# Kernel tuning notes

Measured on AMD Instinct MI355X. Metric: run time of the kernel, lower is better.

Reference implementation:

```python
import jax, jax.numpy as jnp
import numpy as np

N, E, E_LBL = 50000, 800000, 200000
D_IN, H = 128, 128


def setup_inputs() -> dict:
    key = jax.random.key(0)
    ks = jax.random.split(key, 12)
    s = 0.05
    return {
        "x": jax.random.normal(ks[0], (N, D_IN), jnp.float32),
        "edge_index": jax.random.randint(ks[1], (2, E), 0, N, jnp.int64),
        "edge_label_index": jax.random.randint(ks[2], (2, E_LBL), 0, N, jnp.int64),
        "pre_w": jax.random.normal(ks[3], (D_IN, H), jnp.float32) * s,
        "pre_b": jax.random.normal(ks[4], (H,), jnp.float32) * s,
        "Wx": jax.random.normal(ks[5], (3, 2, H, H), jnp.float32) * s,  # gates z,r,h x cheb orders T0,T1
        "bx": jax.random.normal(ks[6], (3, H), jnp.float32) * s,
        "Wh": jax.random.normal(ks[7], (3, 2, H, H), jnp.float32) * s,
        "bh": jax.random.normal(ks[8], (3, H), jnp.float32) * s,
        "post_w": jax.random.normal(ks[9], (H, 2), jnp.float32) * s,
        "post_b": jax.random.normal(ks[10], (2,), jnp.float32) * s,
    }


def reference(x, edge_index, edge_label_index, pre_w, pre_b, Wx, bx, Wh, bh, post_w, post_b):
    n = x.shape[0]
    src, dst = edge_index[0], edge_index[1]

    # Scaled Chebyshev Laplacian (sym norm, lambda_max=2): L_hat = -D^{-1/2} A D^{-1/2}
    # (diagonal of L_hat is exactly 0, so only off-diagonal edge terms remain).
    deg = jax.ops.segment_sum(jnp.ones_like(src, dtype=x.dtype), src, num_segments=n)
    dinv = jnp.where(deg > 0, jax.lax.rsqrt(jnp.maximum(deg, 1.0)), 0.0)
    w = -(dinv[src] * dinv[dst])  # [E]

    def lap(v):  # L_hat @ v : gather src rows, weight, scatter-add at dst
        return jax.ops.segment_sum(w[:, None] * v[src], dst, num_segments=n)

    def cheb(v, Lv, W2, b):  # ChebConv K=2: T0(v)@W0 + T1(v)@W1 + b
        return v @ W2[0] + Lv @ W2[1] + b

    # pre: Linear(input_dim -> hidden)
    Xh = x @ pre_w + pre_b  # [N, H]
    LX = lap(Xh)

    # GConvGRU single step, H0 = 0
    Hc = jnp.zeros_like(Xh)
    LH = lap(Hc)
    Z = jax.nn.sigmoid(cheb(Xh, LX, Wx[0], bx[0]) + cheb(Hc, LH, Wh[0], bh[0]))
    R = jax.nn.sigmoid(cheb(Xh, LX, Wx[1], bx[1]) + cheb(Hc, LH, Wh[1], bh[1]))
    HR = Hc * R
    LHR = lap(HR)
    Ht = jnp.tanh(cheb(Xh, LX, Wx[2], bx[2]) + cheb(HR, LHR, Wh[2], bh[2]))
    Hc = Z * Hc + (1.0 - Z) * Ht

    h = jax.nn.relu(Hc)
    # link decoder: gather endpoints, hadamard, Linear(H->2), sum over logits
    hprod = h[edge_label_index[0]] * h[edge_label_index[1]]  # [E_lbl, H]
    out = hprod @ post_w + post_b  # [E_lbl, 2]
    return jnp.sum(out, axis=-1)  # [E_lbl]
```

## Files before the change

### kernel.cpp

```cpp
#include <hip/hip_runtime.h>
#include <math.h>


#define RND 2048
#define SORT_CAP 1536
#define CAPB 6144

typedef __attribute__((ext_vector_type(4))) float f32x4;
typedef __attribute__((ext_vector_type(8))) short short8;

static __device__ __forceinline__ unsigned short f2b(float f) {
  union { float f; unsigned u; } v; v.f = f;
  unsigned r = (v.u + 0x7fffu + ((v.u >> 16) & 1u)) >> 16;
  return (unsigned short)r;
}
static __device__ __forceinline__ float b2f(unsigned short s) {
  union { unsigned u; float f; } v; v.u = ((unsigned)s) << 16;
  return v.f;
}

__global__ __launch_bounds__(256) void prep_kernel(const float* __restrict__ pre_w, const float* __restrict__ Wx,
                                                   const float* __restrict__ bx, const float* __restrict__ bh,
                                                   const float* __restrict__ post_w, const float* __restrict__ post_b,
                                                   unsigned short* __restrict__ Bt1c, unsigned short* __restrict__ Btc2,
                                                   float* __restrict__ fb2, float* __restrict__ pwsum,
                                                   int* __restrict__ binPos) {
  int e = blockIdx.x * 256 + threadIdx.x;
  if (e < 512) binPos[e] = (e & 255) * CAPB;
  if (e < 16384) {
    int kc = e >> 12, r = e & 4095, col = r >> 5, kk = r & 31;
    Bt1c[e] = f2b(pre_w[(kc * 32 + kk) * 128 + col]);
  }
  int e2 = e - 16384;
  if (e2 >= 0 && e2 < 65536) {
    int kc = e2 >> 13, r = e2 & 8191, cB = r >> 5, kk = r & 31;
    int k = kc * 32 + kk, half = k >> 7, ki = k & 127;
    int cb = cB >> 7, r7 = cB & 127, nw6 = r7 >> 6, u2 = r7 & 63;
    int g = (u2 >= 32) ? 2 : 0, hcol = cb * 64 + nw6 * 32 + (u2 & 31);
    Btc2[e2] = f2b(Wx[((g * 2 + half) * 128 + ki) * 128 + hcol]);
  }
  int e3 = e - (16384 + 65536);
  if (e3 >= 0 && e3 < 256) {
    int cB = e3;
    int cb = cB >> 7, r7 = cB & 127, nw6 = r7 >> 6, u2 = r7 & 63;
    int g = (u2 >= 32) ? 2 : 0, hcol = cb * 64 + nw6 * 32 + (u2 & 31);
    fb2[cB] = bx[g * 128 + hcol] + bh[g * 128 + hcol];
  }
  int e4 = e - (16384 + 65536 + 256);
  if (e4 >= 0 && e4 < 128) pwsum[e4] = post_w[2 * e4] + post_w[2 * e4 + 1];
  if (e4 == 128) pwsum[128] = post_b[0] + post_b[1];
}

union SMemU {
  struct { unsigned short As[128 * 40]; unsigned short Bs[128 * 40]; } g;
  struct { unsigned ent[RND]; int hist[256], lstart[256], lofs[256], gbase[256], wsum[4];
           unsigned char ebin[RND], sb[RND]; } s;
};

__global__ __launch_bounds__(256) void mega1_kernel(const float* __restrict__ x,
                                                    const unsigned short* __restrict__ Bt1c,
                                                    const float* __restrict__ pre_b,
                                                    unsigned short* __restrict__ Xq,
                                                    const int* __restrict__ ei, int* __restrict__ binPos,
                                                    unsigned* __restrict__ bins,
                                                    unsigned char* __restrict__ sbins,
                                                    int N, int E, int RB) {
  __shared__ SMemU sm;
  const int t = threadIdx.x;

  if ((int)blockIdx.x < RB) {
    unsigned short* As = sm.g.As;
    unsigned short* Bs = sm.g.Bs;
    const int r0 = blockIdx.x * 128;
    const int w = t >> 6, lane = t & 63;
    const int m = lane & 15, q = lane >> 4;
    const int mw = (w >> 1) * 64, nw = (w & 1) * 64;

    f32x4 acc[4][4];
#pragma unroll
    for (int i = 0; i < 4; ++i)
#pragma unroll
      for (int j = 0; j < 4; ++j) acc[i][j] = {0.f, 0.f, 0.f, 0.f};

    const int arow = t >> 1, aseg = t & 1;
    const bool arow_ok = (r0 + arow) < N;
    const float* asrc0 = &x[(size_t)(r0 + arow) * 128 + aseg * 16];

    float4 cav[4]; short8 cbv0, cbv1;
    {
      if (arow_ok) {
#pragma unroll
        for (int i = 0; i < 4; ++i) cav[i] = *(const float4*)(asrc0 + i * 4);
      } else {
#pragma unroll
        for (int i = 0; i < 4; ++i) cav[i] = make_float4(0.f, 0.f, 0.f, 0.f);
      }
      const char* src = (const char*)Bt1c + t * 32;
      cbv0 = *(const short8*)src;
      cbv1 = *(const short8*)(src + 16);
    }

    for (int kc = 0; kc < 4; ++kc) {
      __syncthreads();
      {
        short8 t0, t1;
#pragma unroll
        for (int i = 0; i < 2; ++i) {
          t0[i * 4 + 0] = (short)f2b(cav[i].x); t0[i * 4 + 1] = (short)f2b(cav[i].y);
          t0[i * 4 + 2] = (short)f2b(cav[i].z); t0[i * 4 + 3] = (short)f2b(cav[i].w);
          t1[i * 4 + 0] = (short)f2b(cav[i + 2].x); t1[i * 4 + 1] = (short)f2b(cav[i + 2].y);
          t1[i * 4 + 2] = (short)f2b(cav[i + 2].z); t1[i * 4 + 3] = (short)f2b(cav[i + 2].w);
        }
        *(short8*)&As[arow * 40 + aseg * 16] = t0;
        *(short8*)&As[arow * 40 + aseg * 16 + 8] = t1;
        int bcol = t >> 1, boff = (t & 1) * 16;
        *(short8*)&Bs[bcol * 40 + boff] = cbv0;
        *(short8*)&Bs[bcol * 40 + boff + 8] = cbv1;
      }
      float4 nav[4]; short8 nbv0, nbv1;
      if (kc < 3) {
        if (arow_ok) {
          const float* src = asrc0 + (kc + 1) * 32;
#pragma unroll
          for (int i = 0; i < 4; ++i) nav[i] = *(const float4*)(src + i * 4);
        } else {
#pragma unroll
          for (int i = 0; i < 4; ++i) nav[i] = make_float4(0.f, 0.f, 0.f, 0.f);
        }
        const char* src = (const char*)Bt1c + (size_t)(kc + 1) * 8192 + t * 32;
        nbv0 = *(const short8*)src;
        nbv1 = *(const short8*)(src + 16);
      }
      __syncthreads();
      short8 af[4], bf[4];
#pragma unroll
      for (int i = 0; i < 4; ++i) af[i] = *(const short8*)&As[(mw + i * 16 + m) * 40 + q * 8];
#pragma unroll
      for (int j = 0; j < 4; ++j) bf[j] = *(const short8*)&Bs[(nw + j * 16 + m) * 40 + q * 8];
#pragma unroll
      for (int i = 0; i < 4; ++i)
#pragma unroll
        for (int j = 0; j < 4; ++j)
          acc[i][j] = __builtin_amdgcn_mfma_f32_16x16x32_bf16(af[i], bf[j], acc[i][j], 0, 0, 0);
      if (kc < 3) {
#pragma unroll
        for (int i = 0; i < 4; ++i) cav[i] = nav[i];
        cbv0 = nbv0; cbv1 = nbv1;
      }
    }

#pragma unroll
    for (int i = 0; i < 4; ++i) {
      int rb2 = r0 + mw + i * 16 + q * 4;
#pragma unroll
      for (int j = 0; j < 4; ++j) {
        int col = nw + j * 16 + m;
        float bias = pre_b[col];
#pragma unroll
        for (int r = 0; r < 4; ++r) {
          int row = rb2 + r;
          if (row < N) Xq[(size_t)row * 128 + col] = f2b(acc[i][j][r] + bias);
        }
      }
    }
    return;
  }

  unsigned* ent = sm.s.ent;
  unsigned char* ebin = sm.s.ebin;
  unsigned char* sb = sm.s.sb;
  int* hist = sm.s.hist;
  int* lstart = sm.s.lstart;
  int* lofs = sm.s.lofs;
  int* gbase = sm.s.gbase;
  int* wsum = sm.s.wsum;
  const int sbid = (int)blockIdx.x - RB;
  const int snum = (int)gridDim.x - RB;
  const int w = t >> 6, lane = t & 63;
  for (long long base = (long long)sbid * RND; base < E; base += (long long)snum * RND) {
    int cnt = (int)(((long long)E - base < RND) ? (E - base) : RND);
    if (t < 256) hist[t] = 0;
    __syncthreads();
    int my_s[8], my_d[8];
#pragma unroll
    for (int u = 0; u < 8; ++u) {
      int i = u * 256 + t;
      my_s[u] = -1;
      if (i < cnt) {
        int idx = (int)base + i;
        my_s[u] = ei[idx];
        my_d[u] = ei[E + idx];
        atomicAdd(&hist[my_d[u] >> 8], 1);
      }
    }
    __syncthreads();
    {
      int h = hist[t];
      hist[t] = 0;
      int v = h;
#pragma unroll
      for (int dd = 1; dd < 64; dd <<= 1) { int uu = __shfl_up(v, dd); if (lane >= dd) v += uu; }
      if (lane == 63) wsum[w] = v;
      __syncthreads();
      int woff = 0;
#pragma unroll
      for (int ww = 0; ww < 3; ++ww) if (ww < w) woff += wsum[ww];
      int excl = v - h + woff;
      lstart[t] = excl; lofs[t] = excl;
      if (h > 0) gbase[t] = atomicAdd(&binPos[t], h);
    }
    __syncthreads();
#pragma unroll
    for (int u = 0; u < 8; ++u) {
      if (my_s[u] >= 0) {
        int b = my_d[u] >> 8;
        int p = atomicAdd(&lofs[b], 1);
        ent[p] = (unsigned)my_s[u] | ((unsigned)(my_d[u] & 255) << 16);
        ebin[p] = (unsigned char)b;
        atomicAdd(&hist[my_s[u] >> 8], 1);
      }
    }
    __syncthreads();
    for (int i = t; i < cnt; i += 256) {
      int b = ebin[i];
      int pos = gbase[b] + (i - lstart[b]);
      if (pos < (b + 1) * CAPB) bins[pos] = ent[i];
    }
    __syncthreads();
    {
      int h = hist[t];
      int v = h;
#pragma unroll
      for (int dd = 1; dd < 64; dd <<= 1) { int uu = __shfl_up(v, dd); if (lane >= dd) v += uu; }
      if (lane == 63) wsum[w] = v;
      __syncthreads();
      int woff = 0;
#pragma unroll
      for (int ww = 0; ww < 3; ++ww) if (ww < w) woff += wsum[ww];
      int excl = v - h + woff;
      lstart[t] = excl; lofs[t] = excl;
      if (h > 0) gbase[t] = atomicAdd(&binPos[256 + t], h);
    }
    __syncthreads();
#pragma unroll
    for (int u = 0; u < 8; ++u) {
      if (my_s[u] >= 0) {
        int b = my_s[u] >> 8;
        int p = atomicAdd(&lofs[b], 1);
        sb[p] = (unsigned char)(my_s[u] & 255);
        ebin[p] = (unsigned char)b;
      }
    }
    __syncthreads();
    for (int i = t; i < cnt; i += 256) {
      int b = ebin[i];
      int pos = gbase[b] + (i - lstart[b]);
      if (pos < (b + 1) * CAPB) sbins[pos] = sb[i];
    }
    __syncthreads();
  }
}

__global__ __launch_bounds__(256) void deghist_kernel(const unsigned char* __restrict__ sbins,
                                                      const int* __restrict__ binPos,
                                                      int* __restrict__ deg, int N) {
  __shared__ int h[256];
  const int t = threadIdx.x;
  const int bin = blockIdx.x;
  h[t] = 0;
  __syncthreads();
  int T2 = binPos[256 + bin] - bin * CAPB;
  if (T2 > CAPB) T2 = CAPB;
  const unsigned char* __restrict__ p = sbins + (size_t)bin * CAPB;
  for (int i = t; i < T2; i += 256) atomicAdd(&h[p[i]], 1);
  __syncthreads();
  int node = bin * 256 + t;
  if (node < N) deg[node] = h[t];
}

__global__ __launch_bounds__(512) void lap_bin_kernel(const unsigned short* __restrict__ Xq,
                                                      unsigned short* __restrict__ LXc,
                                                      const unsigned* __restrict__ bins,
                                                      const int* __restrict__ binPos,
                                                      const int* __restrict__ deg, int N) {
  __shared__ unsigned eLDS[CAPB];
  __shared__ unsigned short sortS[SORT_CAP];
  __shared__ float sortW[SORT_CAP];
  __shared__ int hist[64], start[64], off[64];
  const int t = threadIdx.x;
  const int bin = blockIdx.x >> 2, qt = blockIdx.x & 3;
  const int lo = bin * CAPB;
  int T = binPos[bin] - lo;
  if (T > CAPB) T = CAPB;
  const unsigned* __restrict__ ebase = &bins[lo];
  if (t < 64) hist[t] = 0;
  __syncthreads();
  for (int i = t; i < T; i += 512) {
    unsigned e = ebase[i];
    eLDS[i] = e;
    int dl = (e >> 16) & 255;
    if ((dl >> 6) == qt) atomicAdd(&hist[dl & 63], 1);
  }
  __syncthreads();
  if (t < 64) {
    int h = hist[t];
    int v = h;
#pragma unroll
    for (int d = 1; d < 64; d <<= 1) {
      int u = __shfl_up(v, d);
      if (t >= d) v += u;
    }
    start[t] = v - h;
    off[t] = v - h;
  }
  __syncthreads();
  for (int i = t; i < T; i += 512) {
    unsigned e = eLDS[i];
    int dl = (e >> 16) & 255;
    if ((dl >> 6) == qt) {
      int s = (int)(e & 0xFFFFu);
      int p = atomicAdd(&off[dl & 63], 1);
      if (p < SORT_CAP) {
        int dg = deg[s];
        sortS[p] = (unsigned short)s;
        sortW[p] = dg > 0 ? rsqrtf((float)dg) : 0.0f;
      }
    }
  }
  __syncthreads();
  const int wv = t >> 6, lane = t & 63;
  for (int n = wv; n < 64; n += 8) {
    int node = bin * 256 + qt * 64 + n;
    if (node >= N) break;
    int st = start[n], cnum = hist[n];
    float ax = 0.f, ay = 0.f;
    for (int j = 0; j < cnum; j += 8) {
      unsigned v[8]; float ws[8];
#pragma unroll
      for (int u = 0; u < 8; ++u) {
        int idx = j + u;
        int s = 0; float w = 0.f;
        if (idx < cnum) { s = sortS[st + idx]; w = sortW[st + idx]; }
        ws[u] = w;
        v[u] = *(const unsigned*)((const char*)Xq + (size_t)s * 256 + lane * 4);
      }
#pragma unroll
      for (int u = 0; u < 8; ++u) {
        union { unsigned u32; float f; } fl, fh;
        fl.u32 = v[u] << 16; fh.u32 = v[u] & 0xffff0000u;
        ax += ws[u] * fl.f;
        ay += ws[u] * fh.f;
      }
    }
    int dgn = deg[node];
    float wd = dgn > 0 ? -rsqrtf((float)dgn) : 0.0f;
    unsigned o = (unsigned)f2b(ax * wd) | ((unsigned)f2b(ay * wd) << 16);
    *(unsigned*)((char*)LXc + (size_t)node * 256 + lane * 4) = o;
  }
}

__global__ __launch_bounds__(256) void gemm2_mfma(const unsigned short* __restrict__ Xq,
                                                  const unsigned short* __restrict__ LXc,
                                                  const unsigned short* __restrict__ Btc2,
                                                  const float* __restrict__ fb2,
                                                  unsigned short* __restrict__ hb, int N) {
  __shared__ unsigned short As[128 * 40];
  __shared__ unsigned short Bs[128 * 40];
  const int t = threadIdx.x;
  const int rb = blockIdx.x >> 1, cb = blockIdx.x & 1;
  const int r0 = rb * 128;
  const int w = t >> 6, lane = t & 63;
  const int m = lane & 15, q = lane >> 4;
  const int mw = (w >> 1) * 64, nw = (w & 1) * 64;

  f32x4 acc[4][4];
#pragma unroll
  for (int i = 0; i < 4; ++i)
#pragma unroll
    for (int j = 0; j < 4; ++j) acc[i][j] = {0.f, 0.f, 0.f, 0.f};

  const int arow = t >> 1;
  const int aoff = (t & 1) * 32;
  const char* aXq = (const char*)Xq + (size_t)(r0 + arow) * 256 + aoff;
  const char* aLX = (const char*)LXc + (size_t)(r0 + arow) * 256 + aoff;
  const char* bsrc0 = (const char*)Btc2 + (size_t)cb * 8192 + t * 32;

  short8 cav0, cav1, cbv0, cbv1;
  cav0 = *(const short8*)aXq;
  cav1 = *(const short8*)(aXq + 16);
  cbv0 = *(const short8*)bsrc0;
  cbv1 = *(const short8*)(bsrc0 + 16);

  for (int kc = 0; kc < 8; ++kc) {
    __syncthreads();
    *(short8*)&As[arow * 40 + (aoff >> 1)] = cav0;
    *(short8*)&As[arow * 40 + (aoff >> 1) + 8] = cav1;
    {
      int bcol = t >> 1, boff = (t & 1) * 16;
      *(short8*)&Bs[bcol * 40 + boff] = cbv0;
      *(short8*)&Bs[bcol * 40 + boff + 8] = cbv1;
    }
    short8 nav0, nav1, nbv0, nbv1;
    if (kc < 7) {
      int kn = kc + 1;
      const char* asrc = (kn < 4) ? (aXq + kn * 64) : (aLX + (kn - 4) * 64);
      nav0 = *(const short8*)asrc;
      nav1 = *(const short8*)(asrc + 16);
      const char* bsrc = bsrc0 + (size_t)kn * 16384;
      nbv0 = *(const short8*)bsrc;
      nbv1 = *(const short8*)(bsrc + 16);
    }
    __syncthreads();
    short8 af[4], bf[4];
#pragma unroll
    for (int i = 0; i < 4; ++i) af[i] = *(const short8*)&As[(mw + i * 16 + m) * 40 + q * 8];
#pragma unroll
    for (int j = 0; j < 4; ++j) bf[j] = *(const short8*)&Bs[(nw + j * 16 + m) * 40 + q * 8];
#pragma unroll
    for (int i = 0; i < 4; ++i)
#pragma unroll
      for (int j = 0; j < 4; ++j)
        acc[i][j] = __builtin_amdgcn_mfma_f32_16x16x32_bf16(af[i], bf[j], acc[i][j], 0, 0, 0);
    if (kc < 7) { cav0 = nav0; cav1 = nav1; cbv0 = nbv0; cbv1 = nbv1; }
  }

#pragma unroll
  for (int i = 0; i < 4; ++i) {
    int rbase = r0 + mw + i * 16 + q * 4;
#pragma unroll
    for (int jz = 0; jz < 2; ++jz) {
      int cBz = cb * 128 + nw + jz * 16 + m;
      int hc = cb * 64 + (nw >> 1) + jz * 16 + m;
      float bz = fb2[cBz], bt = fb2[cBz + 32];
#pragma unroll
      for (int r = 0; r < 4; ++r) {
        int row = rbase + r;
        if (row < N) {
          float zp = acc[i][jz][r] + bz;
          float tp = acc[i][jz + 2][r] + bt;
          float zs = 1.0f / (1.0f + __expf(-zp));
          float th = tanhf(tp);
          hb[(size_t)row * 128 + hc] = f2b(fmaxf((1.0f - zs) * th, 0.0f));
        }
      }
    }
  }
}

__global__ __launch_bounds__(256) void decoder_kernel(const unsigned short* __restrict__ hb,
                                                      const int* __restrict__ eli,
                                                      const float* __restrict__ pwsum, float* __restrict__ out, int M) {
  int t = threadIdx.x;
  int i = blockIdx.x * 16 + (t >> 4);
  int l = t & 15;
  if (i >= M) return;
  int a = eli[i], b = eli[M + i];
  int k = l * 8;
  short8 va = *(const short8*)&hb[(size_t)a * 128 + k];
  short8 vb = *(const short8*)&hb[(size_t)b * 128 + k];
  const float4* pwp = (const float4*)&pwsum[k];
  float4 p0 = pwp[0], p1 = pwp[1];
  float s = 0.0f;
  s += b2f((unsigned short)va[0]) * b2f((unsigned short)vb[0]) * p0.x;
  s += b2f((unsigned short)va[1]) * b2f((unsigned short)vb[1]) * p0.y;
  s += b2f((unsigned short)va[2]) * b2f((unsigned short)vb[2]) * p0.z;
  s += b2f((unsigned short)va[3]) * b2f((unsigned short)vb[3]) * p0.w;
  s += b2f((unsigned short)va[4]) * b2f((unsigned short)vb[4]) * p1.x;
  s += b2f((unsigned short)va[5]) * b2f((unsigned short)vb[5]) * p1.y;
  s += b2f((unsigned short)va[6]) * b2f((unsigned short)vb[6]) * p1.z;
  s += b2f((unsigned short)va[7]) * b2f((unsigned short)vb[7]) * p1.w;
#pragma unroll
  for (int off = 8; off; off >>= 1) s += __shfl_xor(s, off);
  if (l == 0) out[i] = s + pwsum[128];
}

extern "C" void kernel_launch(void* const* d_in, const int* in_sizes, int n_in,
                              void* d_out, int out_size, void* d_ws, size_t ws_size,
                              hipStream_t stream) {
  const float* x      = (const float*)d_in[0];
  const int*   ei     = (const int*)d_in[1];
  const int*   eli    = (const int*)d_in[2];
  const float* pre_w  = (const float*)d_in[3];
  const float* pre_b  = (const float*)d_in[4];
  const float* Wx     = (const float*)d_in[5];
  const float* bx     = (const float*)d_in[6];
  const float* bh     = (const float*)d_in[8];
  const float* post_w = (const float*)d_in[9];
  const float* post_b = (const float*)d_in[10];
  float* out = (float*)d_out;

  const int N = in_sizes[0] / 128;
  const int E = in_sizes[1] / 2;
  const int M = in_sizes[2] / 2;
  const int RB = (N + 127) / 128;
  const int NBIN = (N + 255) / 256;
  const int SCAT = (E + RND - 1) / RND;

  char* W = (char*)d_ws;
  size_t o = 0;
  int* deg = (int*)(W + o);       o += (size_t)N * 4;
  int* binPos = (int*)(W + o);    o += 2048;
  o = (o + 255) & ~(size_t)255;
  unsigned* bins = (unsigned*)(W + o); o += (size_t)NBIN * CAPB * 4;
  o = (o + 255) & ~(size_t)255;
  unsigned char* sbins = (unsigned char*)(W + o); o += (size_t)NBIN * CAPB;
  o = (o + 255) & ~(size_t)255;
  unsigned short* Xq = (unsigned short*)(W + o);  o += (size_t)RB * 128 * 256;
  unsigned short* LXc = (unsigned short*)(W + o); o += (size_t)RB * 128 * 256;
  unsigned short* hb = (unsigned short*)(W + o);  o += (size_t)N * 256;
  unsigned short* Bt1c = (unsigned short*)(W + o); o += 32768;
  unsigned short* Btc2 = (unsigned short*)(W + o); o += 131072;
  float* fb2 = (float*)(W + o);  o += 1024;
  float* pwsum = (float*)(W + o); o += 768;

  prep_kernel<<<322, 256, 0, stream>>>(pre_w, Wx, bx, bh, post_w, post_b, Bt1c, Btc2, fb2, pwsum,
                                       binPos);
  mega1_kernel<<<RB + SCAT, 256, 0, stream>>>(x, Bt1c, pre_b, Xq, ei, binPos, bins, sbins, N, E, RB);
  deghist_kernel<<<NBIN, 256, 0, stream>>>(sbins, binPos, deg, N);
  lap_bin_kernel<<<NBIN * 4, 512, 0, stream>>>(Xq, LXc, bins, binPos, deg, N);
  gemm2_mfma<<<RB * 2, 256, 0, stream>>>(Xq, LXc, Btc2, fb2, hb, N);
  decoder_kernel<<<(M + 15) / 16, 256, 0, stream>>>(hb, eli, pwsum, out, M);
}
```

Baseline: 199.3 us.

## Prescale X by source dinv in deghist and vectorize laplacian gather

The degree-histogram kernel now computes negative inverse-sqrt degrees and writes a copy of Xq with each row scaled by its source node's dinv. That removes the per-edge deg lookup and rsqrt from the laplacian's sort phase. The laplacian gather now loads 16-byte vectors and handles four edges per wave at once, combined with a cross-lane shuffle reduction. The cost is an extra N×256-byte bf16 buffer written and read, plus a second bf16 rounding of the scaled features.

```diff
diff --git a/kernel.cpp b/kernel.cpp
--- a/kernel.cpp
+++ b/kernel.cpp
@@ -8,6 +8,7 @@
 
 typedef __attribute__((ext_vector_type(4))) float f32x4;
 typedef __attribute__((ext_vector_type(8))) short short8;
+typedef __attribute__((ext_vector_type(4))) unsigned u32x4;
 
 static __device__ __forceinline__ unsigned short f2b(float f) {
   union { float f; unsigned u; } v; v.f = f;
@@ -261,31 +262,57 @@
   }
 }
 
-__global__ __launch_bounds__(256) void deghist_kernel(const unsigned char* __restrict__ sbins,
+__global__ __launch_bounds__(512) void deghist_kernel(const unsigned char* __restrict__ sbins,
                                                       const int* __restrict__ binPos,
-                                                      int* __restrict__ deg, int N) {
+                                                      const unsigned short* __restrict__ Xq,
+                                                      unsigned short* __restrict__ Xs,
+                                                      float* __restrict__ dinvNeg, int N) {
   __shared__ int h[256];
+  __shared__ float sdi[256];
   const int t = threadIdx.x;
   const int bin = blockIdx.x;
-  h[t] = 0;
+  if (t < 256) h[t] = 0;
   __syncthreads();
   int T2 = binPos[256 + bin] - bin * CAPB;
   if (T2 > CAPB) T2 = CAPB;
   const unsigned char* __restrict__ p = sbins + (size_t)bin * CAPB;
-  for (int i = t; i < T2; i += 256) atomicAdd(&h[p[i]], 1);
-  __syncthreads();
-  int node = bin * 256 + t;
-  if (node < N) deg[node] = h[t];
-}
-
-__global__ __launch_bounds__(512) void lap_bin_kernel(const unsigned short* __restrict__ Xq,
+  for (int i = t; i < T2; i += 512) atomicAdd(&h[p[i]], 1);
+  __syncthreads();
+  if (t < 256) {
+    int node = bin * 256 + t;
+    float di = h[t] > 0 ? rsqrtf((float)h[t]) : 0.0f;
+    sdi[t] = di;
+    if (node < N) dinvNeg[node] = -di;
+  }
+  __syncthreads();
+  const int wv = t >> 6, lane = t & 63;
+  const int g4 = lane >> 4, sl = lane & 15;
+#pragma unroll
+  for (int it = 0; it < 8; ++it) {
+    int r = wv * 32 + it * 4 + g4;
+    int rnode = bin * 256 + r;
+    if (rnode < N) {
+      float di_r = sdi[r];
+      u32x4 v = *(const u32x4*)((const char*)Xq + (size_t)rnode * 256 + sl * 16);
+      u32x4 o;
+#pragma unroll
+      for (int k = 0; k < 4; ++k) {
+        union { unsigned u32; float f; } fl, fh;
+        fl.u32 = v[k] << 16; fh.u32 = v[k] & 0xffff0000u;
+        o[k] = (unsigned)f2b(fl.f * di_r) | ((unsigned)f2b(fh.f * di_r) << 16);
+      }
+      *(u32x4*)((char*)Xs + (size_t)rnode * 256 + sl * 16) = o;
+    }
+  }
+}
+
+__global__ __launch_bounds__(512) void lap_bin_kernel(const unsigned short* __restrict__ Xs,
                                                       unsigned short* __restrict__ LXc,
                                                       const unsigned* __restrict__ bins,
                                                       const int* __restrict__ binPos,
-                                                      const int* __restrict__ deg, int N) {
+                                                      const float* __restrict__ dinvNeg, int N) {
   __shared__ unsigned eLDS[CAPB];
   __shared__ unsigned short sortS[SORT_CAP];
-  __shared__ float sortW[SORT_CAP];
   __shared__ int hist[64], start[64], off[64];
   const int t = threadIdx.x;
   const int bin = blockIdx.x >> 2, qt = blockIdx.x & 3;
@@ -318,44 +345,49 @@
     unsigned e = eLDS[i];
     int dl = (e >> 16) & 255;
     if ((dl >> 6) == qt) {
-      int s = (int)(e & 0xFFFFu);
       int p = atomicAdd(&off[dl & 63], 1);
-      if (p < SORT_CAP) {
-        int dg = deg[s];
-        sortS[p] = (unsigned short)s;
-        sortW[p] = dg > 0 ? rsqrtf((float)dg) : 0.0f;
-      }
+      if (p < SORT_CAP) sortS[p] = (unsigned short)(e & 0xFFFFu);
     }
   }
   __syncthreads();
   const int wv = t >> 6, lane = t & 63;
+  const int g4 = lane >> 4, sl = lane & 15;
   for (int n = wv; n < 64; n += 8) {
     int node = bin * 256 + qt * 64 + n;
     if (node >= N) break;
     int st = start[n], cnum = hist[n];
-    float ax = 0.f, ay = 0.f;
+    float acc[8] = {0.f, 0.f, 0.f, 0.f, 0.f, 0.f, 0.f, 0.f};
     for (int j = 0; j < cnum; j += 8) {
-      unsigned v[8]; float ws[8];
-#pragma unroll
-      for (int u = 0; u < 8; ++u) {
-        int idx = j + u;
-        int s = 0; float w = 0.f;
-        if (idx < cnum) { s = sortS[st + idx]; w = sortW[st + idx]; }
-        ws[u] = w;
-        v[u] = *(const unsigned*)((const char*)Xq + (size_t)s * 256 + lane * 4);
-      }
-#pragma unroll
-      for (int u = 0; u < 8; ++u) {
-        union { unsigned u32; float f; } fl, fh;
-        fl.u32 = v[u] << 16; fh.u32 = v[u] & 0xffff0000u;
-        ax += ws[u] * fl.f;
-        ay += ws[u] * fh.f;
-      }
-    }
-    int dgn = deg[node];
-    float wd = dgn > 0 ? -rsqrtf((float)dgn) : 0.0f;
-    unsigned o = (unsigned)f2b(ax * wd) | ((unsigned)f2b(ay * wd) << 16);
-    *(unsigned*)((char*)LXc + (size_t)node * 256 + lane * 4) = o;
+#pragma unroll
+      for (int u = 0; u < 2; ++u) {
+        int idx = j + u * 4 + g4;
+        bool val = idx < cnum;
+        int s = sortS[st + (val ? idx : 0)];
+        u32x4 vv = *(const u32x4*)((const char*)Xs + (size_t)s * 256 + sl * 16);
+        if (val) {
+#pragma unroll
+          for (int k = 0; k < 4; ++k) {
+            union { unsigned u32; float f; } fl, fh;
+            fl.u32 = vv[k] << 16; fh.u32 = vv[k] & 0xffff0000u;
+            acc[2 * k] += fl.f;
+            acc[2 * k + 1] += fh.f;
+          }
+        }
+      }
+    }
+#pragma unroll
+    for (int k = 0; k < 8; ++k) {
+      acc[k] += __shfl_xor(acc[k], 16);
+      acc[k] += __shfl_xor(acc[k], 32);
+    }
+    if (g4 == 0) {
+      float wd = dinvNeg[node];
+      u32x4 o;
+#pragma unroll
+      for (int k = 0; k < 4; ++k)
+        o[k] = (unsigned)f2b(acc[2 * k] * wd) | ((unsigned)f2b(acc[2 * k + 1] * wd) << 16);
+      *(u32x4*)((char*)LXc + (size_t)node * 256 + sl * 16) = o;
+    }
   }
 }
 
@@ -498,7 +530,7 @@
 
   char* W = (char*)d_ws;
   size_t o = 0;
-  int* deg = (int*)(W + o);       o += (size_t)N * 4;
+  float* dinvNeg = (float*)(W + o); o += (size_t)N * 4;
   int* binPos = (int*)(W + o);    o += 2048;
   o = (o + 255) & ~(size_t)255;
   unsigned* bins = (unsigned*)(W + o); o += (size_t)NBIN * CAPB * 4;
@@ -506,6 +538,7 @@
   unsigned char* sbins = (unsigned char*)(W + o); o += (size_t)NBIN * CAPB;
   o = (o + 255) & ~(size_t)255;
   unsigned short* Xq = (unsigned short*)(W + o);  o += (size_t)RB * 128 * 256;
+  unsigned short* Xs = (unsigned short*)(W + o);  o += (size_t)RB * 128 * 256;
   unsigned short* LXc = (unsigned short*)(W + o); o += (size_t)RB * 128 * 256;
   unsigned short* hb = (unsigned short*)(W + o);  o += (size_t)N * 256;
   unsigned short* Bt1c = (unsigned short*)(W + o); o += 32768;
@@ -516,8 +549,8 @@
   prep_kernel<<<322, 256, 0, stream>>>(pre_w, Wx, bx, bh, post_w, post_b, Bt1c, Btc2, fb2, pwsum,
                                        binPos);
   mega1_kernel<<<RB + SCAT, 256, 0, stream>>>(x, Bt1c, pre_b, Xq, ei, binPos, bins, sbins, N, E, RB);
-  deghist_kernel<<<NBIN, 256, 0, stream>>>(sbins, binPos, deg, N);
-  lap_bin_kernel<<<NBIN * 4, 512, 0, stream>>>(Xq, LXc, bins, binPos, deg, N);
+  deghist_kernel<<<NBIN, 512, 0, stream>>>(sbins, binPos, Xq, Xs, dinvNeg, N);
+  lap_bin_kernel<<<NBIN * 4, 512, 0, stream>>>(Xs, LXc, bins, binPos, dinvNeg, N);
   gemm2_mfma<<<RB * 2, 256, 0, stream>>>(Xq, LXc, Btc2, fb2, hb, N);
   decoder_kernel<<<(M + 15) / 16, 256, 0, stream>>>(hb, eli, pwsum, out, M);
 }
```

Result: no change. 197.5 us (-0.9%).
